# Performance work log

Measured on AMD Instinct MI355X. Metric: run time of the kernel, lower is better.

Reference implementation:

```python
import jax, jax.numpy as jnp
import numpy as np
from jax import lax

N = 2048       # number of groups (rows of x)
T = 32768      # total tokens across all ragged segments
D_SEQ = 128    # per-token feature dim
D_LSTM = 512   # RNN hidden per direction (= min(512, d_hidden//2))
D_X = 512      # node feature dim (LazyLinear input)
D_HIDDEN = 2048
D_PROJ = D_HIDDEN - 2 * D_LSTM  # 1024


def setup_inputs() -> dict:
    key = jax.random.key(0)
    ks = jax.random.split(key, 12)
    x = jax.random.normal(ks[0], (N, D_X), jnp.float32)
    seqs = jax.random.normal(ks[1], (T, D_SEQ), jnp.float32)
    # sorted group ids; concat arange(N) to guarantee every group is present
    extra = jax.random.randint(ks[2], (T - N,), 0, N)
    masks = jnp.sort(jnp.concatenate([jnp.arange(N), extra]))
    s = 1.0 / np.sqrt(D_LSTM)
    u = lambda k, shape: jax.random.uniform(k, shape, jnp.float32, -s, s)
    return {
        "x": x, "seqs": seqs, "masks": masks,
        "W_ih_f": u(ks[3], (D_LSTM, D_SEQ)), "W_hh_f": u(ks[4], (D_LSTM, D_LSTM)), "b_f": u(ks[5], (D_LSTM,)),
        "W_ih_b": u(ks[6], (D_LSTM, D_SEQ)), "W_hh_b": u(ks[7], (D_LSTM, D_LSTM)), "b_b": u(ks[8], (D_LSTM,)),
        "Wx": u(ks[9], (D_PROJ, D_X)), "bx": u(ks[10], (D_PROJ,)),
    }


def _dir_scan(pre, starts, W_hh):
    # pre: [T, H] precomputed input projection (+bias); starts: [T] bool segment-start flags.
    # h_t = tanh(pre_t + W_hh h_{t-1}), with h reset to 0 at each segment start.
    def step(h, inp):
        p, st = inp
        h = jnp.tanh(p + jnp.where(st, 0.0, 1.0) * (h @ W_hh.T))
        return h, h
    h0 = jnp.zeros((pre.shape[1],), pre.dtype)
    _, hs = lax.scan(step, h0, (pre, starts))
    return hs  # [T, H]


def reference(x, seqs, masks, W_ih_f, W_hh_f, b_f, W_ih_b, W_hh_b, b_b, Wx, bx):
    # segment boundaries (masks is sorted -> contiguous segments)
    starts = jnp.concatenate([jnp.ones((1,), bool), masks[1:] != masks[:-1]])
    m_rev = masks[::-1]
    starts_rev = jnp.concatenate([jnp.ones((1,), bool), m_rev[1:] != m_rev[:-1]])

    # bidirectional tanh-RNN over each segment (single-layer, like nn.RNN)
    h_f = _dir_scan(seqs @ W_ih_f.T + b_f, starts, W_hh_f)                 # [T, 512]
    h_b = _dir_scan((seqs @ W_ih_b.T + b_b)[::-1], starts_rev, W_hh_b)[::-1]  # [T, 512]
    hidden = jnp.concatenate([h_f, h_b], axis=-1)                           # [T, 1024]

    # mean pool per segment -> one embedding per group
    counts = jax.ops.segment_sum(jnp.ones((masks.shape[0],), hidden.dtype), masks, num_segments=N)
    pooled = jax.ops.segment_sum(hidden, masks, num_segments=N) / counts[:, None]  # [N, 1024]

    # x projection then concat: [x_proj | pooled]
    return jnp.concatenate([x @ Wx.T + bx, pooled], axis=-1)  # [N, 2048]
```

## Files before the change

### kernel.cpp

```cpp
#include <hip/hip_runtime.h>
#include <cstdint>
#include <cstddef>

#define T_N    32768
#define N_SEG  2048
#define DSEQ   128
#define DLSTM  512
#define DX     512
#define DPROJ  1024
#define OUTW   2048
#define WSCALE 2873.6827f
#define SXQ    15.875f
#define LOG2E2 2.8853900817779268f
#define DEQH   (2.8853900817779268f/(2873.6827f*127.0f))
#define MAGICF 12582912.0f
#define MAGIC_C (12582912.0f + 127.0f)

typedef __attribute__((ext_vector_type(8))) short short8;
typedef __attribute__((ext_vector_type(4))) float f32x4;
typedef __attribute__((ext_vector_type(4))) int i32x4;

#if __has_builtin(__builtin_amdgcn_exp2f)
#define EXP2F(x) __builtin_amdgcn_exp2f(x)
#else
#define EXP2F(x) __expf((x) * 0.6931471805599453f)
#endif
#if __has_builtin(__builtin_amdgcn_rcpf)
#define RCPF(x) __builtin_amdgcn_rcpf(x)
#else
#define RCPF(x) (1.0f / (x))
#endif

#define PIN(x) asm volatile("" : "+v"(x))

__device__ inline unsigned int cvtpk(float a, float b) {
  unsigned int r;
  asm("v_cvt_pk_bf16_f32 %0, %1, %2" : "=v"(r) : "v"(a), "v"(b));
  return r;
}

__device__ inline unsigned pack4(unsigned b0, unsigned b1, unsigned b2, unsigned b3) {
#if __has_builtin(__builtin_amdgcn_perm)
  unsigned lo = __builtin_amdgcn_perm(b1, b0, 0x00000400u);
  unsigned hi = __builtin_amdgcn_perm(b3, b2, 0x00000400u);
  return __builtin_amdgcn_perm(hi, lo, 0x05040100u);
#else
  return (b0 & 255u) | ((b1 & 255u) << 8) | ((b2 & 255u) << 16) | (b3 << 24);
#endif
}

__global__ __launch_bounds__(256) void prep_kernel(
    const int* __restrict__ masks,
    const float* __restrict__ Whh_f, const float* __restrict__ Whh_b,
    const float* __restrict__ Wih_f, const float* __restrict__ Wih_b,
    signed char* __restrict__ W8, signed char* __restrict__ WX8,
    int* __restrict__ seg_start, int* __restrict__ seg_end,
    int* __restrict__ tile_ctr) {
  const int bid = blockIdx.x, tid = threadIdx.x;
  if (bid == 0 && tid == 0) *tile_ctr = 0;
  if (bid < 128) {
    int t = bid * 256 + tid;
    int m = masks[t];
    if (t == 0 || masks[t - 1] != m) seg_start[m] = t;
    if (t == T_N - 1 || masks[t + 1] != m) seg_end[m] = t + 1;
  } else if (bid < 256) {
    int id = (bid - 128) * 256 + tid;
    int lane = id & 63;
    int kt = (id >> 6) & 7;
    int mt = (id >> 9) & 1;
    int wv = (id >> 10) & 15;
    int dir = id >> 14;
    int n = wv * 32 + mt * 16 + (lane & 15);
    int k0 = kt * 64 + (lane >> 4) * 16;
    const float* wp = (dir ? Whh_b : Whh_f) + (size_t)n * DLSTM + k0;
    signed char pkt[16];
#pragma unroll
    for (int q = 0; q < 4; ++q) {
      float4 v = *(const float4*)(wp + q * 4);
      float vv[4] = {v.x, v.y, v.z, v.w};
#pragma unroll
      for (int j = 0; j < 4; ++j) {
        int qq = (int)rintf(vv[j] * WSCALE);
        qq = qq > 127 ? 127 : (qq < -127 ? -127 : qq);
        pkt[q * 4 + j] = (signed char)qq;
      }
    }
    i32x4 v16;
    __builtin_memcpy(&v16, pkt, 16);
    *(i32x4*)&W8[(size_t)id * 16] = v16;
  } else {
    int id = (bid - 256) * 256 + tid;
    int lane = id & 63;
    int kt = (id >> 6) & 1;
    int mt = (id >> 7) & 1;
    int wv = (id >> 8) & 15;
    int dir = id >> 12;
    int n = wv * 32 + mt * 16 + (lane & 15);
    int k0 = kt * 64 + (lane >> 4) * 16;
    const float* wp = (dir ? Wih_b : Wih_f) + (size_t)n * DSEQ + k0;
    signed char pkt[16];
#pragma unroll
    for (int q = 0; q < 4; ++q) {
      float4 v = *(const float4*)(wp + q * 4);
      float vv[4] = {v.x, v.y, v.z, v.w};
#pragma unroll
      for (int j = 0; j < 4; ++j) {
        int qq = (int)rintf(vv[j] * WSCALE);
        qq = qq > 127 ? 127 : (qq < -127 ? -127 : qq);
        pkt[q * 4 + j] = (signed char)qq;
      }
    }
    i32x4 v16;
    __builtin_memcpy(&v16, pkt, 16);
    *(i32x4*)&WX8[(size_t)id * 16] = v16;
  }
}

__global__ __launch_bounds__(1024, 4) void fused_kernel(
    const float* __restrict__ seqs,
    const signed char* __restrict__ W8, const signed char* __restrict__ WX8,
    const int* __restrict__ seg_start, const int* __restrict__ seg_end,
    const float* __restrict__ b_f, const float* __restrict__ b_b,
    const float* __restrict__ x, const float* __restrict__ Wx,
    const float* __restrict__ bx, float* __restrict__ out,
    int* __restrict__ tile_ctr) {
  __shared__ __align__(16) char smem[36880];
  const int bid = blockIdx.x, tid = threadIdx.x;
  const int wv = tid >> 6, lane = tid & 63;

  {
    const int dir = bid & 1, bb = bid >> 1;
    const int chain = lane & 15, kgrp = lane >> 4;
    const int dbase = wv << 5;
    signed char* H = (signed char*)smem;
    signed char* Xs = (signed char*)(smem + 16896);
    int* meta = (int*)(smem + 21504);

    if (tid < 16) {
      int st = seg_start[bb * 16 + tid];
      meta[tid] = st;
      meta[16 + tid] = seg_end[bb * 16 + tid] - st;
    }
    {
      int r = tid >> 6, o = lane << 3;
      *(uint2*)(H + r * 528 + o) = make_uint2(0u, 0u);
    }

    i32x4 w[2][8], wx[2][2];
    {
      const signed char* wb = W8 + ((size_t)((dir << 4) + wv) << 14) + (lane << 4);
#pragma unroll
      for (int mt = 0; mt < 2; ++mt)
#pragma unroll
        for (int kt = 0; kt < 8; ++kt)
          w[mt][kt] = *(const i32x4*)(wb + (mt * 8 + kt) * 1024);
      const signed char* wxb = WX8 + ((size_t)((dir << 4) + wv) << 12) + (lane << 4);
#pragma unroll
      for (int mt = 0; mt < 2; ++mt)
#pragma unroll
        for (int kt = 0; kt < 2; ++kt)
          wx[mt][kt] = *(const i32x4*)(wxb + (mt * 2 + kt) * 1024);
    }
#pragma unroll
    for (int mt = 0; mt < 2; ++mt) {
#pragma unroll
      for (int kt = 0; kt < 8; ++kt) PIN(w[mt][kt]);
      PIN(wx[mt][0]); PIN(wx[mt][1]);
    }

    float bsc[2][4];
    {
      const float* bsrc = dir ? b_b : b_f;
#pragma unroll
      for (int mt = 0; mt < 2; ++mt) {
        float4 u = *(const float4*)(bsrc + dbase + mt * 16 + (kgrp << 2));
        bsc[mt][0] = u.x * LOG2E2; bsc[mt][1] = u.y * LOG2E2;
        bsc[mt][2] = u.z * LOG2E2; bsc[mt][3] = u.w * LOG2E2;
      }
    }
    __syncthreads();

    int maxlen = 0;
#pragma unroll
    for (int c = 0; c < 16; ++c) {
      int l = meta[16 + c];
      maxlen = maxlen > l ? maxlen : l;
    }
    const int myLen = meta[16 + chain];
    const int stStart = meta[wv], stLen = meta[16 + wv];
    const int jx = lane << 1;

    {
      int t0 = dir ? (stStart + stLen - 1) : stStart;
      float2 xv0 = *(const float2*)(seqs + (size_t)t0 * DSEQ + jx);
      unsigned c0 = __float_as_uint(fminf(fmaxf(xv0.x * SXQ, -127.f), 127.f) + MAGICF);
      unsigned c1 = __float_as_uint(fminf(fmaxf(xv0.y * SXQ, -127.f), 127.f) + MAGICF);
      *(unsigned short*)(Xs + wv * 144 + jx) =
          (unsigned short)((c0 & 255u) | ((c1 & 255u) << 8));
    }
    __syncthreads();

    float pool[2][4];
#pragma unroll
    for (int mt = 0; mt < 2; ++mt)
#pragma unroll
      for (int r = 0; r < 4; ++r) pool[mt][r] = 0.f;

    int cur = 0;
    for (int s = 0; s < maxlen; ++s) {
      int sn = (s + 1 < stLen) ? (s + 1) : (stLen - 1);
      int tn = dir ? (stStart + stLen - 1 - sn) : (stStart + sn);
      float2 xv = *(const float2*)(seqs + (size_t)tn * DSEQ + jx);

      i32x4 acc[2], ax[2];
#pragma unroll
      for (int mt = 0; mt < 2; ++mt) {
        acc[mt] = (i32x4){0, 0, 0, 0};
        ax[mt] = (i32x4){0, 0, 0, 0};
      }
      {
        const signed char* xr = Xs + cur * 2304 + chain * 144;
#pragma unroll
        for (int kt = 0; kt < 2; ++kt) {
          i32x4 xb = *(const i32x4*)(xr + kt * 64 + (kgrp << 4));
#pragma unroll
          for (int mt = 0; mt < 2; ++mt)
            ax[mt] = __builtin_amdgcn_mfma_i32_16x16x64_i8(wx[mt][kt], xb, ax[mt], 0, 0, 0);
        }
        const signed char* hr = H + cur * 8448 + chain * 528;
#pragma unroll
        for (int kt = 0; kt < 8; ++kt) {
          i32x4 hb = *(const i32x4*)(hr + kt * 64 + (kgrp << 4));
#pragma unroll
          for (int mt = 0; mt < 2; ++mt)
            acc[mt] = __builtin_amdgcn_mfma_i32_16x16x64_i8(w[mt][kt], hb, acc[mt], 0, 0, 0);
        }
      }

      const float msk = (s < myLen) ? 1.f : 0.f;
#pragma unroll
      for (int mt = 0; mt < 2; ++mt) {
        unsigned b[4];
#pragma unroll
        for (int r = 0; r < 4; ++r) {
          int comb = acc[mt][r] + (ax[mt][r] << 3);
          float x2 = fmaf((float)comb, DEQH, bsc[mt][r]);
          float e = EXP2F(x2);
          float rc = RCPF(e + 1.f);
          pool[mt][r] = fmaf(rc, msk, pool[mt][r]);
          b[r] = __float_as_uint(fmaf(-254.f, rc, MAGIC_C));
        }
        *(unsigned*)(H + (cur ^ 1) * 8448 + chain * 528 + dbase + mt * 16 + (kgrp << 2)) =
            pack4(b[0], b[1], b[2], b[3]);
      }
      {
        unsigned c0 = __float_as_uint(fminf(fmaxf(xv.x * SXQ, -127.f), 127.f) + MAGICF);
        unsigned c1 = __float_as_uint(fminf(fmaxf(xv.y * SXQ, -127.f), 127.f) + MAGICF);
        *(unsigned short*)(Xs + (cur ^ 1) * 2304 + wv * 144 + jx) =
            (unsigned short)((c0 & 255u) | ((c1 & 255u) << 8));
      }
      asm volatile("s_waitcnt lgkmcnt(0)" ::: "memory");
      __builtin_amdgcn_s_barrier();
      __builtin_amdgcn_sched_barrier(0);
      cur ^= 1;
    }

    const int sid = bb * 16 + chain;
    const float s2 = -2.0f / (float)myLen;
    float* op = out + (size_t)sid * OUTW + DPROJ + dir * DLSTM + dbase + (kgrp << 2);
#pragma unroll
    for (int mt = 0; mt < 2; ++mt)
      *(float4*)(op + mt * 16) =
          make_float4(fmaf(s2, pool[mt][0], 1.f), fmaf(s2, pool[mt][1], 1.f),
                      fmaf(s2, pool[mt][2], 1.f), fmaf(s2, pool[mt][3], 1.f));
  }

  {
    int* tileslot = (int*)(smem + 36864);
    unsigned short (*As)[72] = (unsigned short(*)[72])smem;
    unsigned short (*Bs)[72] = (unsigned short(*)[72])(smem + 18432);
    const int rowA = lane & 15, kgrp = lane >> 4;
    const int wm = (wv >> 2) << 5, wn = (wv & 3) << 5;
    const int srow = tid >> 3, skc = (tid & 7) << 2;

    for (;;) {
      __syncthreads();
      if (tid == 0) *tileslot = atomicAdd(tile_ctr, 1);
      __syncthreads();
      const int tile = *tileslot;
      if (tile >= 128) break;
      const int m0 = (tile >> 3) << 7, n0 = (tile & 7) << 7;

      f32x4 acc[2][2];
#pragma unroll
      for (int i = 0; i < 2; ++i)
#pragma unroll
        for (int j = 0; j < 2; ++j) acc[i][j] = (f32x4){0.f, 0.f, 0.f, 0.f};

      for (int k0 = 0; k0 < DX; k0 += 32) {
        __syncthreads();
        {
          float4 va = *(const float4*)(x + (size_t)(m0 + srow) * DX + k0 + skc);
          unsigned wa[2] = {cvtpk(va.x, va.y), cvtpk(va.z, va.w)};
          *(uint2*)&As[srow][skc] = *(uint2*)wa;
          float4 vb = *(const float4*)(Wx + (size_t)(n0 + srow) * DX + k0 + skc);
          unsigned wb2[2] = {cvtpk(vb.x, vb.y), cvtpk(vb.z, vb.w)};
          *(uint2*)&Bs[srow][skc] = *(uint2*)wb2;
        }
        __syncthreads();
        short8 af[2], bf[2];
#pragma unroll
        for (int mt = 0; mt < 2; ++mt)
          af[mt] = *(const short8*)&As[wm + mt * 16 + rowA][kgrp << 3];
#pragma unroll
        for (int nt = 0; nt < 2; ++nt)
          bf[nt] = *(const short8*)&Bs[wn + nt * 16 + rowA][kgrp << 3];
#pragma unroll
        for (int mt = 0; mt < 2; ++mt)
#pragma unroll
          for (int nt = 0; nt < 2; ++nt)
            acc[mt][nt] = __builtin_amdgcn_mfma_f32_16x16x32_bf16(af[mt], bf[nt], acc[mt][nt], 0, 0, 0);
      }

#pragma unroll
      for (int mt = 0; mt < 2; ++mt)
#pragma unroll
        for (int nt = 0; nt < 2; ++nt) {
          int n = n0 + wn + nt * 16 + rowA;
          float bv = bx[n];
#pragma unroll
          for (int r = 0; r < 4; ++r) {
            int m = m0 + wm + mt * 16 + (kgrp << 2) + r;
            out[(size_t)m * OUTW + n] = acc[mt][nt][r] + bv;
          }
        }
    }
  }
}

extern "C" void kernel_launch(void* const* d_in, const int* in_sizes, int n_in,
                              void* d_out, int out_size, void* d_ws, size_t ws_size,
                              hipStream_t stream) {
  const float* x     = (const float*)d_in[0];
  const float* seqs  = (const float*)d_in[1];
  const int*   masks = (const int*)d_in[2];
  const float* Wih_f = (const float*)d_in[3];
  const float* Whh_f = (const float*)d_in[4];
  const float* b_f   = (const float*)d_in[5];
  const float* Wih_b = (const float*)d_in[6];
  const float* Whh_b = (const float*)d_in[7];
  const float* b_b   = (const float*)d_in[8];
  const float* Wx    = (const float*)d_in[9];
  const float* bx    = (const float*)d_in[10];
  float* out = (float*)d_out;

  char* ws = (char*)d_ws;
  signed char* W8  = (signed char*)ws;
  signed char* WX8 = (signed char*)(ws + (size_t)512 * 1024);
  int* seg_start = (int*)(ws + (size_t)640 * 1024);
  int* seg_end   = seg_start + N_SEG;
  int* tile_ctr  = seg_end + N_SEG;

  prep_kernel<<<288, 256, 0, stream>>>(masks, Whh_f, Whh_b, Wih_f, Wih_b,
                                       W8, WX8, seg_start, seg_end, tile_ctr);
  fused_kernel<<<256, 1024, 0, stream>>>(seqs, W8, WX8, seg_start, seg_end,
                                         b_f, b_b, x, Wx, bx, out, tile_ctr);
}
```

Before: 75.64 us.

## Move x-projection GEMM into prep kernel, leaving scan kernel RNN-only

The dense x@Wx^T+bx GEMM moves out of the tail of the fused scan kernel into 128 extra blocks of the prep kernel. Those blocks use 128x128 tiles with 4x4 MFMA tiles per wave and a software float-to-bf16 conversion. The scan kernel now only runs the RNN recurrence and pooling, with lower shared-memory use and waves_per_eu 4. This drops the atomic tile counter and the serialised GEMM that ran after the scan. The cost is a longer prep kernel that runs before the scan starts, and a more expensive bf16 conversion.

New measurement: 85.54 us. 1.13x slower.

```diff
diff --git a/kernel.cpp b/kernel.cpp
--- a/kernel.cpp
+++ b/kernel.cpp
@@ -33,10 +33,10 @@
 
 #define PIN(x) asm volatile("" : "+v"(x))
 
-__device__ inline unsigned int cvtpk(float a, float b) {
-  unsigned int r;
-  asm("v_cvt_pk_bf16_f32 %0, %1, %2" : "=v"(r) : "v"(a), "v"(b));
-  return r;
+__device__ inline unsigned short f2b(float f) {
+  unsigned int u = __float_as_uint(f);
+  unsigned int r = (u + 0x7FFFu + ((u >> 16) & 1u)) >> 16;
+  return (unsigned short)r;
 }
 
 __device__ inline unsigned pack4(unsigned b0, unsigned b1, unsigned b2, unsigned b3) {
@@ -55,9 +55,10 @@
     const float* __restrict__ Wih_f, const float* __restrict__ Wih_b,
     signed char* __restrict__ W8, signed char* __restrict__ WX8,
     int* __restrict__ seg_start, int* __restrict__ seg_end,
-    int* __restrict__ tile_ctr) {
+    const float* __restrict__ x, const float* __restrict__ Wx,
+    const float* __restrict__ bx, float* __restrict__ out) {
+  __shared__ __align__(16) char smem[20608];
   const int bid = blockIdx.x, tid = threadIdx.x;
-  if (bid == 0 && tid == 0) *tile_ctr = 0;
   if (bid < 128) {
     int t = bid * 256 + tid;
     int m = masks[t];
@@ -88,7 +89,7 @@
     i32x4 v16;
     __builtin_memcpy(&v16, pkt, 16);
     *(i32x4*)&W8[(size_t)id * 16] = v16;
-  } else {
+  } else if (bid < 288) {
     int id = (bid - 256) * 256 + tid;
     int lane = id & 63;
     int kt = (id >> 6) & 1;
@@ -113,229 +114,230 @@
     i32x4 v16;
     __builtin_memcpy(&v16, pkt, 16);
     *(i32x4*)&WX8[(size_t)id * 16] = v16;
-  }
-}
-
-__global__ __launch_bounds__(1024, 4) void fused_kernel(
+  } else {
+    const int pb_ = bid - 288;
+    const int m0 = (pb_ >> 3) << 7, n0 = (pb_ & 7) << 7;
+    unsigned short (*As)[40] = (unsigned short(*)[40])smem;
+    unsigned short (*Bs)[40] = (unsigned short(*)[40])(smem + 10240);
+    const int wave = tid >> 6, lane = tid & 63;
+    const int wm = (wave >> 1) << 6, wn = (wave & 1) << 6;
+    const int rowA = lane & 15, kgrp = lane >> 4;
+    const int lrow = tid >> 1, lkc = (tid & 1) << 4;
+
+    f32x4 acc[4][4];
+#pragma unroll
+    for (int i = 0; i < 4; ++i)
+#pragma unroll
+      for (int j = 0; j < 4; ++j) acc[i][j] = (f32x4){0.f, 0.f, 0.f, 0.f};
+
+    for (int k0 = 0; k0 < DX; k0 += 32) {
+      __syncthreads();
+      {
+        const float* ap = x + (size_t)(m0 + lrow) * DX + k0 + lkc;
+        unsigned short pa[16];
+#pragma unroll
+        for (int q = 0; q < 4; ++q) {
+          float4 v = *(const float4*)(ap + q * 4);
+          pa[q * 4 + 0] = f2b(v.x); pa[q * 4 + 1] = f2b(v.y);
+          pa[q * 4 + 2] = f2b(v.z); pa[q * 4 + 3] = f2b(v.w);
+        }
+        *(short8*)&As[lrow][lkc] = *(short8*)&pa[0];
+        *(short8*)&As[lrow][lkc + 8] = *(short8*)&pa[8];
+
+        const float* bp = Wx + (size_t)(n0 + lrow) * DX + k0 + lkc;
+        unsigned short pb2[16];
+#pragma unroll
+        for (int q = 0; q < 4; ++q) {
+          float4 v = *(const float4*)(bp + q * 4);
+          pb2[q * 4 + 0] = f2b(v.x); pb2[q * 4 + 1] = f2b(v.y);
+          pb2[q * 4 + 2] = f2b(v.z); pb2[q * 4 + 3] = f2b(v.w);
+        }
+        *(short8*)&Bs[lrow][lkc] = *(short8*)&pb2[0];
+        *(short8*)&Bs[lrow][lkc + 8] = *(short8*)&pb2[8];
+      }
+      __syncthreads();
+      short8 af[4], bf[4];
+#pragma unroll
+      for (int mt = 0; mt < 4; ++mt) af[mt] = *(const short8*)&As[wm + mt * 16 + rowA][kgrp << 3];
+#pragma unroll
+      for (int nt = 0; nt < 4; ++nt) bf[nt] = *(const short8*)&Bs[wn + nt * 16 + rowA][kgrp << 3];
+#pragma unroll
+      for (int mt = 0; mt < 4; ++mt)
+#pragma unroll
+        for (int nt = 0; nt < 4; ++nt)
+          acc[mt][nt] = __builtin_amdgcn_mfma_f32_16x16x32_bf16(af[mt], bf[nt], acc[mt][nt], 0, 0, 0);
+    }
+
+#pragma unroll
+    for (int mt = 0; mt < 4; ++mt)
+#pragma unroll
+      for (int nt = 0; nt < 4; ++nt) {
+        int n = n0 + wn + nt * 16 + rowA;
+        float bv = bx[n];
+#pragma unroll
+        for (int r = 0; r < 4; ++r) {
+          int m = m0 + wm + mt * 16 + (kgrp << 2) + r;
+          out[(size_t)m * OUTW + n] = acc[mt][nt][r] + bv;
+        }
+      }
+  }
+}
+
+__global__ __attribute__((amdgpu_waves_per_eu(4, 4))) __launch_bounds__(1024)
+void scan_kernel(
     const float* __restrict__ seqs,
     const signed char* __restrict__ W8, const signed char* __restrict__ WX8,
     const int* __restrict__ seg_start, const int* __restrict__ seg_end,
     const float* __restrict__ b_f, const float* __restrict__ b_b,
-    const float* __restrict__ x, const float* __restrict__ Wx,
-    const float* __restrict__ bx, float* __restrict__ out,
-    int* __restrict__ tile_ctr) {
-  __shared__ __align__(16) char smem[36880];
+    float* __restrict__ out) {
+  __shared__ __align__(16) char smem[21760];
   const int bid = blockIdx.x, tid = threadIdx.x;
   const int wv = tid >> 6, lane = tid & 63;
 
+  const int dir = bid & 1, bb = bid >> 1;
+  const int chain = lane & 15, kgrp = lane >> 4;
+  const int dbase = wv << 5;
+  signed char* H = (signed char*)smem;
+  signed char* Xs = (signed char*)(smem + 16896);
+  int* meta = (int*)(smem + 21504);
+
+  if (tid < 16) {
+    int st = seg_start[bb * 16 + tid];
+    meta[tid] = st;
+    meta[16 + tid] = seg_end[bb * 16 + tid] - st;
+  }
   {
-    const int dir = bid & 1, bb = bid >> 1;
-    const int chain = lane & 15, kgrp = lane >> 4;
-    const int dbase = wv << 5;
-    signed char* H = (signed char*)smem;
-    signed char* Xs = (signed char*)(smem + 16896);
-    int* meta = (int*)(smem + 21504);
-
-    if (tid < 16) {
-      int st = seg_start[bb * 16 + tid];
-      meta[tid] = st;
-      meta[16 + tid] = seg_end[bb * 16 + tid] - st;
+    int r = tid >> 6, o = lane << 3;
+    *(uint2*)(H + r * 528 + o) = make_uint2(0u, 0u);
+  }
+
+  i32x4 w[2][8], wx[2][2];
+  {
+    const signed char* wb = W8 + ((size_t)((dir << 4) + wv) << 14) + (lane << 4);
+#pragma unroll
+    for (int mt = 0; mt < 2; ++mt)
+#pragma unroll
+      for (int kt = 0; kt < 8; ++kt)
+        w[mt][kt] = *(const i32x4*)(wb + (mt * 8 + kt) * 1024);
+    const signed char* wxb = WX8 + ((size_t)((dir << 4) + wv) << 12) + (lane << 4);
+#pragma unroll
+    for (int mt = 0; mt < 2; ++mt)
+#pragma unroll
+      for (int kt = 0; kt < 2; ++kt)
+        wx[mt][kt] = *(const i32x4*)(wxb + (mt * 2 + kt) * 1024);
+  }
+#pragma unroll
+  for (int mt = 0; mt < 2; ++mt) {
+#pragma unroll
+    for (int kt = 0; kt < 8; ++kt) PIN(w[mt][kt]);
+    PIN(wx[mt][0]); PIN(wx[mt][1]);
+  }
+
+  float bsc[2][4];
+  {
+    const float* bsrc = dir ? b_b : b_f;
+#pragma unroll
+    for (int mt = 0; mt < 2; ++mt) {
+      float4 u = *(const float4*)(bsrc + dbase + mt * 16 + (kgrp << 2));
+      bsc[mt][0] = u.x * LOG2E2; bsc[mt][1] = u.y * LOG2E2;
+      bsc[mt][2] = u.z * LOG2E2; bsc[mt][3] = u.w * LOG2E2;
+    }
+  }
+  __syncthreads();
+
+  int maxlen = 0;
+#pragma unroll
+  for (int c = 0; c < 16; ++c) {
+    int l = meta[16 + c];
+    maxlen = maxlen > l ? maxlen : l;
+  }
+  const int myLen = meta[16 + chain];
+  const int stStart = meta[wv], stLen = meta[16 + wv];
+  const int jx = lane << 1;
+
+  {
+    int t0 = dir ? (stStart + stLen - 1) : stStart;
+    float2 xv0 = *(const float2*)(seqs + (size_t)t0 * DSEQ + jx);
+    unsigned c0 = __float_as_uint(fminf(fmaxf(xv0.x * SXQ, -127.f), 127.f) + MAGICF);
+    unsigned c1 = __float_as_uint(fminf(fmaxf(xv0.y * SXQ, -127.f), 127.f) + MAGICF);
+    *(unsigned short*)(Xs + wv * 144 + jx) =
+        (unsigned short)((c0 & 255u) | ((c1 & 255u) << 8));
+  }
+  __syncthreads();
+
+  float pool[2][4];
+#pragma unroll
+  for (int mt = 0; mt < 2; ++mt)
+#pragma unroll
+    for (int r = 0; r < 4; ++r) pool[mt][r] = 0.f;
+
+  int cur = 0;
+  for (int s = 0; s < maxlen; ++s) {
+    int sn = (s + 1 < stLen) ? (s + 1) : (stLen - 1);
+    int tn = dir ? (stStart + stLen - 1 - sn) : (stStart + sn);
+    float2 xv = *(const float2*)(seqs + (size_t)tn * DSEQ + jx);
+
+    i32x4 acc[2], ax[2];
+#pragma unroll
+    for (int mt = 0; mt < 2; ++mt) {
+      acc[mt] = (i32x4){0, 0, 0, 0};
+      ax[mt] = (i32x4){0, 0, 0, 0};
     }
     {
-      int r = tid >> 6, o = lane << 3;
-      *(uint2*)(H + r * 528 + o) = make_uint2(0u, 0u);
-    }
-
-    i32x4 w[2][8], wx[2][2];
+      const signed char* xr = Xs + cur * 2304 + chain * 144;
+#pragma unroll
+      for (int kt = 0; kt < 2; ++kt) {
+        i32x4 xb = *(const i32x4*)(xr + kt * 64 + (kgrp << 4));
+#pragma unroll
+        for (int mt = 0; mt < 2; ++mt)
+          ax[mt] = __builtin_amdgcn_mfma_i32_16x16x64_i8(wx[mt][kt], xb, ax[mt], 0, 0, 0);
+      }
+      const signed char* hr = H + cur * 8448 + chain * 528;
+#pragma unroll
+      for (int kt = 0; kt < 8; ++kt) {
+        i32x4 hb = *(const i32x4*)(hr + kt * 64 + (kgrp << 4));
+#pragma unroll
+        for (int mt = 0; mt < 2; ++mt)
+          acc[mt] = __builtin_amdgcn_mfma_i32_16x16x64_i8(w[mt][kt], hb, acc[mt], 0, 0, 0);
+      }
+    }
+
+    const float msk = (s < myLen) ? 1.f : 0.f;
+#pragma unroll
+    for (int mt = 0; mt < 2; ++mt) {
+      unsigned b[4];
+#pragma unroll
+      for (int r = 0; r < 4; ++r) {
+        int comb = acc[mt][r] + (ax[mt][r] << 3);
+        float x2 = fmaf((float)comb, DEQH, bsc[mt][r]);
+        float e = EXP2F(x2);
+        float rc = RCPF(e + 1.f);
+        pool[mt][r] = fmaf(rc, msk, pool[mt][r]);
+        b[r] = __float_as_uint(fmaf(-254.f, rc, MAGIC_C));
+      }
+      *(unsigned*)(H + (cur ^ 1) * 8448 + chain * 528 + dbase + mt * 16 + (kgrp << 2)) =
+          pack4(b[0], b[1], b[2], b[3]);
+    }
     {
-      const signed char* wb = W8 + ((size_t)((dir << 4) + wv) << 14) + (lane << 4);
-#pragma unroll
-      for (int mt = 0; mt < 2; ++mt)
-#pragma unroll
-        for (int kt = 0; kt < 8; ++kt)
-          w[mt][kt] = *(const i32x4*)(wb + (mt * 8 + kt) * 1024);
-      const signed char* wxb = WX8 + ((size_t)((dir << 4) + wv) << 12) + (lane << 4);
-#pragma unroll
-      for (int mt = 0; mt < 2; ++mt)
-#pragma unroll
-        for (int kt = 0; kt < 2; ++kt)
-          wx[mt][kt] = *(const i32x4*)(wxb + (mt * 2 + kt) * 1024);
-    }
-#pragma unroll
-    for (int mt = 0; mt < 2; ++mt) {
-#pragma unroll
-      for (int kt = 0; kt < 8; ++kt) PIN(w[mt][kt]);
-      PIN(wx[mt][0]); PIN(wx[mt][1]);
-    }
-
-    float bsc[2][4];
-    {
-      const float* bsrc = dir ? b_b : b_f;
-#pragma unroll
-      for (int mt = 0; mt < 2; ++mt) {
-        float4 u = *(const float4*)(bsrc + dbase + mt * 16 + (kgrp << 2));
-        bsc[mt][0] = u.x * LOG2E2; bsc[mt][1] = u.y * LOG2E2;
-        bsc[mt][2] = u.z * LOG2E2; bsc[mt][3] = u.w * LOG2E2;
-      }
-    }
-    __syncthreads();
-
-    int maxlen = 0;
-#pragma unroll
-    for (int c = 0; c < 16; ++c) {
-      int l = meta[16 + c];
-      maxlen = maxlen > l ? maxlen : l;
-    }
-    const int myLen = meta[16 + chain];
-    const int stStart = meta[wv], stLen = meta[16 + wv];
-    const int jx = lane << 1;
-
-    {
-      int t0 = dir ? (stStart + stLen - 1) : stStart;
-      float2 xv0 = *(const float2*)(seqs + (size_t)t0 * DSEQ + jx);
-      unsigned c0 = __float_as_uint(fminf(fmaxf(xv0.x * SXQ, -127.f), 127.f) + MAGICF);
-      unsigned c1 = __float_as_uint(fminf(fmaxf(xv0.y * SXQ, -127.f), 127.f) + MAGICF);
-      *(unsigned short*)(Xs + wv * 144 + jx) =
+      unsigned c0 = __float_as_uint(fminf(fmaxf(xv.x * SXQ, -127.f), 127.f) + MAGICF);
+      unsigned c1 = __float_as_uint(fminf(fmaxf(xv.y * SXQ, -127.f), 127.f) + MAGICF);
+      *(unsigned short*)(Xs + (cur ^ 1) * 2304 + wv * 144 + jx) =
           (unsigned short)((c0 & 255u) | ((c1 & 255u) << 8));
     }
-    __syncthreads();
-
-    float pool[2][4];
-#pragma unroll
-    for (int mt = 0; mt < 2; ++mt)
-#pragma unroll
-      for (int r = 0; r < 4; ++r) pool[mt][r] = 0.f;
-
-    int cur = 0;
-    for (int s = 0; s < maxlen; ++s) {
-      int sn = (s + 1 < stLen) ? (s + 1) : (stLen - 1);
-      int tn = dir ? (stStart + stLen - 1 - sn) : (stStart + sn);
-      float2 xv = *(const float2*)(seqs + (size_t)tn * DSEQ + jx);
-
-      i32x4 acc[2], ax[2];
-#pragma unroll
-      for (int mt = 0; mt < 2; ++mt) {
-        acc[mt] = (i32x4){0, 0, 0, 0};
-        ax[mt] = (i32x4){0, 0, 0, 0};
-      }
-      {
-        const signed char* xr = Xs + cur * 2304 + chain * 144;
-#pragma unroll
-        for (int kt = 0; kt < 2; ++kt) {
-          i32x4 xb = *(const i32x4*)(xr + kt * 64 + (kgrp << 4));
-#pragma unroll
-          for (int mt = 0; mt < 2; ++mt)
-            ax[mt] = __builtin_amdgcn_mfma_i32_16x16x64_i8(wx[mt][kt], xb, ax[mt], 0, 0, 0);
-        }
-        const signed char* hr = H + cur * 8448 + chain * 528;
-#pragma unroll
-        for (int kt = 0; kt < 8; ++kt) {
-          i32x4 hb = *(const i32x4*)(hr + kt * 64 + (kgrp << 4));
-#pragma unroll
-          for (int mt = 0; mt < 2; ++mt)
-            acc[mt] = __builtin_amdgcn_mfma_i32_16x16x64_i8(w[mt][kt], hb, acc[mt], 0, 0, 0);
-        }
-      }
-
-      const float msk = (s < myLen) ? 1.f : 0.f;
-#pragma unroll
-      for (int mt = 0; mt < 2; ++mt) {
-        unsigned b[4];
-#pragma unroll
-        for (int r = 0; r < 4; ++r) {
-          int comb = acc[mt][r] + (ax[mt][r] << 3);
-          float x2 = fmaf((float)comb, DEQH, bsc[mt][r]);
-          float e = EXP2F(x2);
-          float rc = RCPF(e + 1.f);
-          pool[mt][r] = fmaf(rc, msk, pool[mt][r]);
-          b[r] = __float_as_uint(fmaf(-254.f, rc, MAGIC_C));
-        }
-        *(unsigned*)(H + (cur ^ 1) * 8448 + chain * 528 + dbase + mt * 16 + (kgrp << 2)) =
-            pack4(b[0], b[1], b[2], b[3]);
-      }
-      {
-        unsigned c0 = __float_as_uint(fminf(fmaxf(xv.x * SXQ, -127.f), 127.f) + MAGICF);
-        unsigned c1 = __float_as_uint(fminf(fmaxf(xv.y * SXQ, -127.f), 127.f) + MAGICF);
-        *(unsigned short*)(Xs + (cur ^ 1) * 2304 + wv * 144 + jx) =
-            (unsigned short)((c0 & 255u) | ((c1 & 255u) << 8));
-      }
-      asm volatile("s_waitcnt lgkmcnt(0)" ::: "memory");
-      __builtin_amdgcn_s_barrier();
-      __builtin_amdgcn_sched_barrier(0);
-      cur ^= 1;
-    }
-
-    const int sid = bb * 16 + chain;
-    const float s2 = -2.0f / (float)myLen;
-    float* op = out + (size_t)sid * OUTW + DPROJ + dir * DLSTM + dbase + (kgrp << 2);
-#pragma unroll
-    for (int mt = 0; mt < 2; ++mt)
-      *(float4*)(op + mt * 16) =
-          make_float4(fmaf(s2, pool[mt][0], 1.f), fmaf(s2, pool[mt][1], 1.f),
-                      fmaf(s2, pool[mt][2], 1.f), fmaf(s2, pool[mt][3], 1.f));
-  }
-
-  {
-    int* tileslot = (int*)(smem + 36864);
-    unsigned short (*As)[72] = (unsigned short(*)[72])smem;
-    unsigned short (*Bs)[72] = (unsigned short(*)[72])(smem + 18432);
-    const int rowA = lane & 15, kgrp = lane >> 4;
-    const int wm = (wv >> 2) << 5, wn = (wv & 3) << 5;
-    const int srow = tid >> 3, skc = (tid & 7) << 2;
-
-    for (;;) {
-      __syncthreads();
-      if (tid == 0) *tileslot = atomicAdd(tile_ctr, 1);
-      __syncthreads();
-      const int tile = *tileslot;
-      if (tile >= 128) break;
-      const int m0 = (tile >> 3) << 7, n0 = (tile & 7) << 7;
-
-      f32x4 acc[2][2];
-#pragma unroll
-      for (int i = 0; i < 2; ++i)
-#pragma unroll
-        for (int j = 0; j < 2; ++j) acc[i][j] = (f32x4){0.f, 0.f, 0.f, 0.f};
-
-      for (int k0 = 0; k0 < DX; k0 += 32) {
-        __syncthreads();
-        {
-          float4 va = *(const float4*)(x + (size_t)(m0 + srow) * DX + k0 + skc);
-          unsigned wa[2] = {cvtpk(va.x, va.y), cvtpk(va.z, va.w)};
-          *(uint2*)&As[srow][skc] = *(uint2*)wa;
-          float4 vb = *(const float4*)(Wx + (size_t)(n0 + srow) * DX + k0 + skc);
-          unsigned wb2[2] = {cvtpk(vb.x, vb.y), cvtpk(vb.z, vb.w)};
-          *(uint2*)&Bs[srow][skc] = *(uint2*)wb2;
-        }
-        __syncthreads();
-        short8 af[2], bf[2];
-#pragma unroll
-        for (int mt = 0; mt < 2; ++mt)
-          af[mt] = *(const short8*)&As[wm + mt * 16 + rowA][kgrp << 3];
-#pragma unroll
-        for (int nt = 0; nt < 2; ++nt)
-          bf[nt] = *(const short8*)&Bs[wn + nt * 16 + rowA][kgrp << 3];
-#pragma unroll
-        for (int mt = 0; mt < 2; ++mt)
-#pragma unroll
-          for (int nt = 0; nt < 2; ++nt)
-            acc[mt][nt] = __builtin_amdgcn_mfma_f32_16x16x32_bf16(af[mt], bf[nt], acc[mt][nt], 0, 0, 0);
-      }
-
-#pragma unroll
-      for (int mt = 0; mt < 2; ++mt)
-#pragma unroll
-        for (int nt = 0; nt < 2; ++nt) {
-          int n = n0 + wn + nt * 16 + rowA;
-          float bv = bx[n];
-#pragma unroll
-          for (int r = 0; r < 4; ++r) {
-            int m = m0 + wm + mt * 16 + (kgrp << 2) + r;
-            out[(size_t)m * OUTW + n] = acc[mt][nt][r] + bv;
-          }
-        }
-    }
-  }
+    asm volatile("s_waitcnt lgkmcnt(0)" ::: "memory");
+    __builtin_amdgcn_s_barrier();
+    __builtin_amdgcn_sched_barrier(0);
+    cur ^= 1;
+  }
+
+  const int sid = bb * 16 + chain;
+  const float s2 = -2.0f / (float)myLen;
+  float* op = out + (size_t)sid * OUTW + DPROJ + dir * DLSTM + dbase + (kgrp << 2);
+#pragma unroll
+  for (int mt = 0; mt < 2; ++mt)
+    *(float4*)(op + mt * 16) =
+        make_float4(fmaf(s2, pool[mt][0], 1.f), fmaf(s2, pool[mt][1], 1.f),
+                    fmaf(s2, pool[mt][2], 1.f), fmaf(s2, pool[mt][3], 1.f));
 }
 
 extern "C" void kernel_launch(void* const* d_in, const int* in_sizes, int n_in,
@@ -359,10 +361,10 @@
   signed char* WX8 = (signed char*)(ws + (size_t)512 * 1024);
   int* seg_start = (int*)(ws + (size_t)640 * 1024);
   int* seg_end   = seg_start + N_SEG;
-  int* tile_ctr  = seg_end + N_SEG;
-
-  prep_kernel<<<288, 256, 0, stream>>>(masks, Whh_f, Whh_b, Wih_f, Wih_b,
-                                       W8, WX8, seg_start, seg_end, tile_ctr);
-  fused_kernel<<<256, 1024, 0, stream>>>(seqs, W8, WX8, seg_start, seg_end,
-                                         b_f, b_b, x, Wx, bx, out, tile_ctr);
-}
+
+  prep_kernel<<<416, 256, 0, stream>>>(masks, Whh_f, Whh_b, Wih_f, Wih_b,
+                                       W8, WX8, seg_start, seg_end,
+                                       x, Wx, bx, out);
+  scan_kernel<<<256, 1024, 0, stream>>>(seqs, W8, WX8, seg_start, seg_end,
+                                        b_f, b_b, out);
+}
```
